# Kernel optimization log

Measured on AMD Instinct MI355X. Metric: run time of the kernel, lower is better.

## Reference

```python
import jax, jax.numpy as jnp
import numpy as np

NH, NKV, HD = 8, 1, 256
EPS = 1e-6
SCALE = 1.0 / np.sqrt(HD)


def _rmsnorm(x, w, eps=EPS):
    # Gemma-style: normalize in fp32, scale by raw weight
    xf = x.astype(jnp.float32)
    rms = jax.lax.rsqrt(jnp.mean(xf * xf, axis=-1, keepdims=True) + eps)
    return (xf * rms).astype(x.dtype) * w


def _apply_rope(q, cos, sin):
    # q: (B, H, T, D); cos/sin: (T, D/2)
    half = q.shape[-1] // 2
    q1, q2 = q[..., :half], q[..., half:]
    c = cos[None, None, :, :]
    s = sin[None, None, :, :]
    return jnp.concatenate([q1 * c - q2 * s, q2 * c + q1 * s], axis=-1)


def setup_inputs() -> dict:
    key = jax.random.key(0)
    ks = jax.random.split(key, 8)
    B, T, H = 2, 2048, 1536
    MAXPOS, HALF = 4096, HD // 2
    x = jax.random.normal(ks[0], (B, T, H), dtype=jnp.float32)
    positions = jnp.arange(T, dtype=jnp.int64) if jax.config.jax_enable_x64 else jnp.arange(T, dtype=jnp.int32)
    # real RoPE tables
    inv_freq = 1.0 / (10000.0 ** (np.arange(0, HALF, dtype=np.float32) / HALF))
    ang = np.arange(MAXPOS, dtype=np.float32)[:, None] * inv_freq[None, :]
    cos = jnp.asarray(np.cos(ang))
    sin = jnp.asarray(np.sin(ang))
    # additive causal mask: 0 on/below diag, -1e9 above
    causal_mask = jnp.where(jnp.tril(jnp.ones((T, T), dtype=bool)), 0.0, -1e9).astype(jnp.float32)
    sc = 0.02
    Wq = jax.random.normal(ks[1], (H, NH * HD), dtype=jnp.float32) * sc
    Wk = jax.random.normal(ks[2], (H, NKV * HD), dtype=jnp.float32) * sc
    Wv = jax.random.normal(ks[3], (H, NKV * HD), dtype=jnp.float32) * sc
    Wo = jax.random.normal(ks[4], (NH * HD, H), dtype=jnp.float32) * sc
    q_norm_w = jnp.ones((HD,), dtype=jnp.float32)
    k_norm_w = jnp.ones((HD,), dtype=jnp.float32)
    return {"x": x, "positions": positions, "cos": cos, "sin": sin,
            "causal_mask": causal_mask, "Wq": Wq, "Wk": Wk, "Wv": Wv,
            "Wo": Wo, "q_norm_w": q_norm_w, "k_norm_w": k_norm_w}


def reference(x, positions, cos, sin, causal_mask, Wq, Wk, Wv, Wo, q_norm_w, k_norm_w):
    B, T, _ = x.shape
    q = (x @ Wq).reshape(B, T, NH, HD)
    k = (x @ Wk).reshape(B, T, NKV, HD)
    v = (x @ Wv).reshape(B, T, NKV, HD)
    q = _rmsnorm(q, q_norm_w)
    k = _rmsnorm(k, k_norm_w)
    q = q.transpose(0, 2, 1, 3)  # (B, NH, T, HD)
    k = k.transpose(0, 2, 1, 3)  # (B, NKV, T, HD)
    v = v.transpose(0, 2, 1, 3)
    cos_pos = cos[positions]
    sin_pos = sin[positions]
    q = _apply_rope(q, cos_pos, sin_pos)
    k = _apply_rope(k, cos_pos, sin_pos)
    if NH != NKV:
        n_rep = NH // NKV
        k = jnp.repeat(k, n_rep, axis=1)
        v = jnp.repeat(v, n_rep, axis=1)
    attn = jnp.einsum('bhqd,bhkd->bhqk', q, k) * SCALE
    attn = attn + causal_mask[None, None]
    attn = jax.nn.softmax(attn, axis=-1)
    out = jnp.einsum('bhqk,bhkd->bhqd', attn, v)
    out = out.transpose(0, 2, 1, 3).reshape(B, T, NH * HD)
    return out @ Wo
```

## Files before the change

### kernel.cpp

```cpp
#include <hip/hip_runtime.h>
#include <hip/hip_bf16.h>

typedef __bf16 bf16x8 __attribute__((ext_vector_type(8)));
typedef float  f32x4  __attribute__((ext_vector_type(4)));

__device__ __forceinline__ f32x4 mfma16(bf16x8 a, bf16x8 b, f32x4 c) {
    return __builtin_amdgcn_mfma_f32_16x16x32_bf16(a, b, c, 0, 0, 0);
}

__device__ __forceinline__ void gload_lds16(const void* g, void* l) {
    __builtin_amdgcn_global_load_lds(
        (const __attribute__((address_space(1))) void*)g,
        (__attribute__((address_space(3))) void*)l, 16, 0, 0);
}

__device__ __forceinline__ float bf2f(unsigned short u) {
    unsigned int x = (unsigned int)u << 16;
    return __builtin_bit_cast(float, x);
}
__device__ __forceinline__ unsigned short f2bf(float f) {
    return __builtin_bit_cast(unsigned short, __float2bfloat16(f));
}

#define B_   2
#define T_   2048
#define H_   1536
#define NH_  8
#define HD_  256
#define ND_  2048
#define NQKV 2560

__global__ __launch_bounds__(256) void cvt_f32_bf16(
        const float* __restrict__ src, __hip_bfloat16* __restrict__ dst, int n8) {
    int i = blockIdx.x * 256 + threadIdx.x;
    if (i >= n8) return;
    const float4* s4 = reinterpret_cast<const float4*>(src) + (size_t)i * 2;
    float4 a = s4[0], b = s4[1];
    short4 o0, o1;
    o0.x = (short)f2bf(a.x); o0.y = (short)f2bf(a.y);
    o0.z = (short)f2bf(a.z); o0.w = (short)f2bf(a.w);
    o1.x = (short)f2bf(b.x); o1.y = (short)f2bf(b.y);
    o1.z = (short)f2bf(b.z); o1.w = (short)f2bf(b.w);
    short4* d4 = reinterpret_cast<short4*>(dst) + (size_t)i * 2;
    d4[0] = o0; d4[1] = o1;
}

__global__ __launch_bounds__(256) void transpose_f32_bf16(
        const float* __restrict__ src, __hip_bfloat16* __restrict__ dst,
        int R, int C) {
    __shared__ float tile[32][33];
    int c0 = blockIdx.x * 32, r0 = blockIdx.y * 32;
    int tx = threadIdx.x & 31, ty = threadIdx.x >> 5;
#pragma unroll
    for (int i = 0; i < 32; i += 8)
        tile[ty + i][tx] = src[(size_t)(r0 + ty + i) * C + c0 + tx];
    __syncthreads();
#pragma unroll
    for (int i = 0; i < 32; i += 8)
        dst[(size_t)(c0 + ty + i) * R + r0 + tx] = __float2bfloat16(tile[tx][ty + i]);
}

__global__ __launch_bounds__(256) void transpose_bf16_s(
        const __hip_bfloat16* __restrict__ src, __hip_bfloat16* __restrict__ dst,
        int R, int C, int ss) {
    __shared__ __hip_bfloat16 tile[32][33];
    int c0 = blockIdx.x * 32, r0 = blockIdx.y * 32;
    int tx = threadIdx.x & 31, ty = threadIdx.x >> 5;
#pragma unroll
    for (int i = 0; i < 32; i += 8)
        tile[ty + i][tx] = src[(size_t)(r0 + ty + i) * ss + c0 + tx];
    __syncthreads();
#pragma unroll
    for (int i = 0; i < 32; i += 8)
        dst[(size_t)(c0 + ty + i) * R + r0 + tx] = tile[tx][ty + i];
}

template <bool F32OUT>
__global__ __launch_bounds__(256) void gemm_bt(
        const __hip_bfloat16* __restrict__ A, const __hip_bfloat16* __restrict__ Bt,
        void* __restrict__ Cp, int M, int N, int K) {
    __shared__ char smem[32768];
    const int tid  = threadIdx.x;
    const int lane = tid & 63;
    const int w    = tid >> 6;
    const int wm   = w >> 1, wn = w & 1;
    const int m0   = blockIdx.y * 128, n0 = blockIdx.x * 128;

    f32x4 acc[4][4] = {};

    auto STAGE = [&](int bsel, int k0) {
        char* As = smem + bsel * 16384;
        char* Bs = As + 8192;
#pragma unroll
        for (int it = 0; it < 2; ++it) {
            int o   = it * 4096 + tid * 16;
            int row = o >> 6;
            int cb  = (o & 63) ^ (((o >> 7) & 3) << 4);
            gload_lds16(A  + (size_t)(m0 + row) * K + k0 + (cb >> 1),
                        As + it * 4096 + w * 1024);
            gload_lds16(Bt + (size_t)(n0 + row) * K + k0 + (cb >> 1),
                        Bs + it * 4096 + w * 1024);
        }
    };

    const int nk = K >> 5;
    STAGE(0, 0);
    for (int ik = 0; ik < nk; ++ik) {
        if (ik + 1 < nk) {
            STAGE((ik + 1) & 1, (ik + 1) << 5);
            asm volatile("s_waitcnt vmcnt(4)" ::: "memory");
        } else {
            asm volatile("s_waitcnt vmcnt(0)" ::: "memory");
        }
        __builtin_amdgcn_s_barrier();
        __builtin_amdgcn_sched_barrier(0);

        const char* As = smem + (ik & 1) * 16384;
        const char* Bs = As + 8192;

        bf16x8 af[4], bfr[4];
#pragma unroll
        for (int i = 0; i < 4; ++i) {
            int ar = wm * 64 + i * 16 + (lane & 15);
            int q  = ar * 64 + ((lane >> 4) << 4);
            af[i]  = *(const bf16x8*)(As + (q ^ (((q >> 7) & 3) << 4)));
            int br = wn * 64 + i * 16 + (lane & 15);
            int p  = br * 64 + ((lane >> 4) << 4);
            bfr[i] = *(const bf16x8*)(Bs + (p ^ (((p >> 7) & 3) << 4)));
        }
#pragma unroll
        for (int i = 0; i < 4; ++i)
#pragma unroll
            for (int j = 0; j < 4; ++j)
                acc[i][j] = mfma16(af[i], bfr[j], acc[i][j]);

        if (ik + 1 < nk) __builtin_amdgcn_s_barrier();
    }

#pragma unroll
    for (int i = 0; i < 4; ++i) {
        int rbase = m0 + wm * 64 + i * 16 + ((lane >> 4) << 2);
#pragma unroll
        for (int j = 0; j < 4; ++j) {
            int col = n0 + wn * 64 + j * 16 + (lane & 15);
#pragma unroll
            for (int r = 0; r < 4; ++r) {
                if (F32OUT)
                    ((float*)Cp)[(size_t)(rbase + r) * N + col] = acc[i][j][r];
                else
                    ((__hip_bfloat16*)Cp)[(size_t)(rbase + r) * N + col] =
                        __float2bfloat16(acc[i][j][r]);
            }
        }
    }
}

__global__ __launch_bounds__(256) void norm_rope(
        const __hip_bfloat16* __restrict__ QKV,
        const float* __restrict__ cosT, const float* __restrict__ sinT,
        const int* __restrict__ positions,
        const float* __restrict__ qw, const float* __restrict__ kw,
        __hip_bfloat16* __restrict__ Qn, __hip_bfloat16* __restrict__ Kn) {
    int gw   = blockIdx.x * 4 + (threadIdx.x >> 6);
    int lane = threadIdx.x & 63;
    int bt   = gw / 9;
    int r    = gw - bt * 9;
    int b    = bt >> 11, t = bt & 2047;

    const __hip_bfloat16* src = QKV + (size_t)bt * NQKV + (r < 8 ? r * HD_ : ND_);
    const float* w;
    __hip_bfloat16* dst;
    float sc;
    if (r < 8) {
        w   = qw;
        dst = Qn + (((size_t)(b * NH_ + r) * T_) + t) * HD_;
        sc  = 0.0901684400555590f;
    } else {
        w   = kw;
        dst = Kn + (size_t)bt * HD_;
        sc  = 1.0f;
    }

    short4 raw = *reinterpret_cast<const short4*>(src + lane * 4);
    float v[4];
    v[0] = bf2f((unsigned short)raw.x); v[1] = bf2f((unsigned short)raw.y);
    v[2] = bf2f((unsigned short)raw.z); v[3] = bf2f((unsigned short)raw.w);

    float ss = v[0]*v[0] + v[1]*v[1] + v[2]*v[2] + v[3]*v[3];
#pragma unroll
    for (int d = 1; d < 64; d <<= 1) ss += __shfl_xor(ss, d);
    float rms = rsqrtf(ss * (1.0f / HD_) + 1e-6f);

    int pos = positions[t];
    float4 c4 = *reinterpret_cast<const float4*>(cosT + (size_t)pos * 128 + (lane & 31) * 4);
    float4 s4 = *reinterpret_cast<const float4*>(sinT + (size_t)pos * 128 + (lane & 31) * 4);
    float cv[4] = { c4.x, c4.y, c4.z, c4.w };
    float sv[4] = { s4.x, s4.y, s4.z, s4.w };

    float4 w4 = *reinterpret_cast<const float4*>(w + lane * 4);
    float wv[4] = { w4.x, w4.y, w4.z, w4.w };

    float nf[4], out[4];
#pragma unroll
    for (int j = 0; j < 4; ++j) nf[j] = v[j] * rms * wv[j];
#pragma unroll
    for (int j = 0; j < 4; ++j) {
        float pf = __shfl_xor(nf[j], 32);
        out[j] = (lane < 32) ? (nf[j] * cv[j] - pf * sv[j])
                             : (nf[j] * cv[j] + pf * sv[j]);
    }
    short4 o4;
    o4.x = (short)f2bf(out[0] * sc); o4.y = (short)f2bf(out[1] * sc);
    o4.z = (short)f2bf(out[2] * sc); o4.w = (short)f2bf(out[3] * sc);
    *reinterpret_cast<short4*>(dst + lane * 4) = o4;
}

#define NPAIR 40
__global__ __launch_bounds__(512) void flash_attn_split(
        const __hip_bfloat16* __restrict__ Qn, const __hip_bfloat16* __restrict__ Kn,
        const __hip_bfloat16* __restrict__ Vt,
        __hip_bfloat16* __restrict__ Opart, float* __restrict__ ml) {
    __shared__ char smem[2 * 16384 + 2 * 16384 + 8 * 1536];
    char* Ps = smem + 65536;

    const int tid = threadIdx.x, lane = tid & 63, wid = tid >> 6;
    const int p = blockIdx.x, bh = blockIdx.y;
    const int b = bh >> 3;

    int qt, c;
    if (p < 4)       { qt = p;                   c = 0; }
    else if (p < 12) { qt = 4 + ((p - 4) >> 1);  c = (p - 4) & 1; }
    else if (p < 24) { qt = 8 + (p - 12) / 3;    c = (p - 12) % 3; }
    else             { qt = 12 + ((p - 24) >> 2); c = (p - 24) & 3; }

    const int kv0 = c * 512;
    const int kv1 = min(kv0 + 512, (qt + 1) * 128);
    const int q0  = qt * 128 + wid * 16;
    const int nst = (kv1 - kv0) >> 5;

    const __hip_bfloat16* Qbase = Qn + ((size_t)bh * T_ + q0) * HD_;
    const __hip_bfloat16* Kb    = Kn + (size_t)b * T_ * HD_;
    const __hip_bfloat16* Vb    = Vt + (size_t)b * HD_ * T_;

    bf16x8 qf[8];
#pragma unroll
    for (int ks = 0; ks < 8; ++ks)
        qf[ks] = *(const bf16x8*)(Qbase + (size_t)(lane & 15) * HD_ + ks * 32 +
                                  ((lane >> 4) << 3));

    bf16x8 onesf;
    {
        __bf16 one = (__bf16)1.0f, zro = (__bf16)0.0f;
        __bf16 val = ((lane & 15) == 0) ? one : zro;
#pragma unroll
        for (int i = 0; i < 8; ++i) onesf[i] = val;
    }

    f32x4 acc[16] = {};
    f32x4 accl = {};

    auto STAGE = [&](int bsel, int kbb) {
        char* Kd = smem + bsel * 16384;
        char* Vd = smem + 32768 + bsel * 16384;
#pragma unroll
        for (int it = 0; it < 2; ++it) {
            int o = it * 8192 + tid * 16;
            {
                int row = o >> 9;
                int cb  = (o & 511) ^ ((row & 31) << 4);
                gload_lds16(Kb + (size_t)(kbb + row) * HD_ + (cb >> 1),
                            Kd + it * 8192 + wid * 1024);
            }
            {
                int row = o >> 6;
                int cb  = (o & 63) ^ (((o >> 7) & 3) << 4);
                gload_lds16(Vb + (size_t)row * T_ + kbb + (cb >> 1),
                            Vd + it * 8192 + wid * 1024);
            }
        }
    };

    STAGE(0, kv0);
    for (int i = 0; i < nst; ++i) {
        const int kb = kv0 + (i << 5);
        if (i + 1 < nst) {
            STAGE((i + 1) & 1, kb + 32);
            asm volatile("s_waitcnt vmcnt(4)" ::: "memory");
        } else {
            asm volatile("s_waitcnt vmcnt(0)" ::: "memory");
        }
        __builtin_amdgcn_s_barrier();
        __builtin_amdgcn_sched_barrier(0);

        const char* Ksb = smem + (i & 1) * 16384;
        const char* Vsb = smem + 32768 + (i & 1) * 16384;

        f32x4 s[2] = {};
        __builtin_amdgcn_s_setprio(1);
#pragma unroll
        for (int cf = 0; cf < 2; ++cf) {
#pragma unroll
            for (int ks = 0; ks < 8; ++ks) {
                int krow = cf * 16 + (lane & 15);
                int q    = krow * 512 + ks * 64 + ((lane >> 4) << 4);
                int sw   = q ^ (((q >> 9) & 31) << 4);
                bf16x8 kf = *(const bf16x8*)(Ksb + sw);
                s[cf] = mfma16(qf[ks], kf, s[cf]);
            }
        }
        __builtin_amdgcn_s_setprio(0);

        const bool nm = (kb + 31 > q0);
        __hip_bfloat16* pw = (__hip_bfloat16*)(Ps + wid * 1536);
#pragma unroll
        for (int r = 0; r < 4; ++r) {
            int rw = ((lane >> 4) << 2) + r;
            float s0 = s[0][r], s1 = s[1][r];
            if (nm) {
                int qrow = q0 + rw;
                if (kb + (lane & 15) > qrow)      s0 = -1e30f;
                if (kb + 16 + (lane & 15) > qrow) s1 = -1e30f;
            }
            pw[rw * 48 + (lane & 15)]      = __float2bfloat16(exp2f(s0));
            pw[rw * 48 + 16 + (lane & 15)] = __float2bfloat16(exp2f(s1));
        }

        bf16x8 pf = *(const bf16x8*)(Ps + wid * 1536 + (lane & 15) * 96 +
                                     ((lane >> 4) << 4));
        __builtin_amdgcn_s_setprio(1);
        accl = mfma16(pf, onesf, accl);
#pragma unroll
        for (int nf = 0; nf < 16; ++nf) {
            int vrow = nf * 16 + (lane & 15);
            int q    = vrow * 64 + ((lane >> 4) << 4);
            int sw   = q ^ (((q >> 7) & 3) << 4);
            bf16x8 vf = *(const bf16x8*)(Vsb + sw);
            acc[nf] = mfma16(pf, vf, acc[nf]);
        }
        __builtin_amdgcn_s_setprio(0);

        if (i + 1 < nst) __builtin_amdgcn_s_barrier();
    }

    const int slot = bh * NPAIR + p;
    __hip_bfloat16* ob = Opart + (size_t)slot * (128 * 256);
#pragma unroll
    for (int r = 0; r < 4; ++r) {
        int rw = wid * 16 + ((lane >> 4) << 2) + r;
        __hip_bfloat16* orow = ob + (size_t)rw * 256;
#pragma unroll
        for (int nf = 0; nf < 16; ++nf)
            orow[nf * 16 + (lane & 15)] = __float2bfloat16(acc[nf][r]);
        if ((lane & 15) == 0) ml[slot * 128 + rw] = accl[r];
    }
}

__global__ __launch_bounds__(256) void attn_combine(
        const __hip_bfloat16* __restrict__ Opart, const float* __restrict__ ml,
        __hip_bfloat16* __restrict__ Obuf) {
    const int bid = blockIdx.x;
    const int bh = bid >> 4, qt = bid & 15;
    const int b = bh >> 3, h = bh & 7;

    int ps, np;
    if (qt < 4)       { ps = qt;                 np = 1; }
    else if (qt < 8)  { ps = 4 + 2 * (qt - 4);   np = 2; }
    else if (qt < 12) { ps = 12 + 3 * (qt - 8);  np = 3; }
    else              { ps = 24 + 4 * (qt - 12); np = 4; }
    const int slot0 = bh * NPAIR + ps;

    const int t = threadIdx.x;
    const int row = t >> 1, half = t & 1;

    float L = 0.0f;
    for (int i = 0; i < np; ++i) L += ml[(slot0 + i) * 128 + row];
    float rL = 1.0f / L;

    __hip_bfloat16* orow = Obuf + ((size_t)(b * T_ + qt * 128 + row)) * ND_ +
                           h * HD_ + half * 128;
#pragma unroll
    for (int cc = 0; cc < 16; ++cc) {
        float a[8] = {0,0,0,0,0,0,0,0};
        for (int i = 0; i < np; ++i) {
            const __hip_bfloat16* pr = Opart + (size_t)(slot0 + i) * (128 * 256) +
                                       (size_t)row * 256 + half * 128 + cc * 8;
            short4 v0 = *reinterpret_cast<const short4*>(pr);
            short4 v1 = *reinterpret_cast<const short4*>(pr + 4);
            a[0] += bf2f((unsigned short)v0.x);
            a[1] += bf2f((unsigned short)v0.y);
            a[2] += bf2f((unsigned short)v0.z);
            a[3] += bf2f((unsigned short)v0.w);
            a[4] += bf2f((unsigned short)v1.x);
            a[5] += bf2f((unsigned short)v1.y);
            a[6] += bf2f((unsigned short)v1.z);
            a[7] += bf2f((unsigned short)v1.w);
        }
        short4 o0, o1;
        o0.x = (short)f2bf(a[0] * rL); o0.y = (short)f2bf(a[1] * rL);
        o0.z = (short)f2bf(a[2] * rL); o0.w = (short)f2bf(a[3] * rL);
        o1.x = (short)f2bf(a[4] * rL); o1.y = (short)f2bf(a[5] * rL);
        o1.z = (short)f2bf(a[6] * rL); o1.w = (short)f2bf(a[7] * rL);
        *reinterpret_cast<short4*>(orow + cc * 8)     = o0;
        *reinterpret_cast<short4*>(orow + cc * 8 + 4) = o1;
    }
}

extern "C" void kernel_launch(void* const* d_in, const int* in_sizes, int n_in,
                              void* d_out, int out_size, void* d_ws, size_t ws_size,
                              hipStream_t stream) {
    const float* x    = (const float*)d_in[0];
    const int*   pos  = (const int*)d_in[1];
    const float* cosT = (const float*)d_in[2];
    const float* sinT = (const float*)d_in[3];
    const float* Wq = (const float*)d_in[5];
    const float* Wk = (const float*)d_in[6];
    const float* Wv = (const float*)d_in[7];
    const float* Wo = (const float*)d_in[8];
    const float* qw = (const float*)d_in[9];
    const float* kw = (const float*)d_in[10];

    char* ws0 = (char*)d_ws;
    __hip_bfloat16* WqkvT  = (__hip_bfloat16*)(ws0 + 0);
    __hip_bfloat16* xb     = (__hip_bfloat16*)(ws0 + 7864320);
    __hip_bfloat16* QKVraw = (__hip_bfloat16*)(ws0 + 20447232);
    __hip_bfloat16* Opart  = (__hip_bfloat16*)(ws0 + 0);
    float*          ml     = (float*)(ws0 + 41943040);
    __hip_bfloat16* WoT    = (__hip_bfloat16*)(ws0 + 42598400);
    __hip_bfloat16* Qn     = (__hip_bfloat16*)(ws0 + 48889856);
    __hip_bfloat16* Obuf   = Qn;
    __hip_bfloat16* Kn     = (__hip_bfloat16*)(ws0 + 65667072);
    __hip_bfloat16* Vt     = (__hip_bfloat16*)(ws0 + 67764224);
    float* out = (float*)d_out;

    const int MT = B_ * T_;

    cvt_f32_bf16<<<(MT * H_ / 8 + 255) / 256, 256, 0, stream>>>(x, xb, MT * H_ / 8);

    transpose_f32_bf16<<<dim3(ND_ / 32, H_ / 32), 256, 0, stream>>>(
        Wq, WqkvT, H_, ND_);
    transpose_f32_bf16<<<dim3(HD_ / 32, H_ / 32), 256, 0, stream>>>(
        Wk, WqkvT + (size_t)ND_ * H_, H_, HD_);
    transpose_f32_bf16<<<dim3(HD_ / 32, H_ / 32), 256, 0, stream>>>(
        Wv, WqkvT + (size_t)(ND_ + HD_) * H_, H_, HD_);
    transpose_f32_bf16<<<dim3(H_ / 32, ND_ / 32), 256, 0, stream>>>(
        Wo, WoT, ND_, H_);

    gemm_bt<false><<<dim3(NQKV / 128, MT / 128), 256, 0, stream>>>(
        xb, WqkvT, QKVraw, MT, NQKV, H_);

    norm_rope<<<(MT * 9) / 4, 256, 0, stream>>>(
        QKVraw, cosT, sinT, pos, qw, kw, Qn, Kn);

    for (int b = 0; b < B_; ++b)
        transpose_bf16_s<<<dim3(HD_ / 32, T_ / 32), 256, 0, stream>>>(
            QKVraw + (size_t)b * T_ * NQKV + ND_ + HD_,
            Vt + (size_t)b * HD_ * T_, T_, HD_, NQKV);

    flash_attn_split<<<dim3(NPAIR, B_ * NH_), 512, 0, stream>>>(
        Qn, Kn, Vt, Opart, ml);
    attn_combine<<<B_ * NH_ * 16, 256, 0, stream>>>(Opart, ml, Obuf);

    gemm_bt<true><<<dim3(H_ / 128, MT / 128), 256, 0, stream>>>(
        Obuf, WoT, out, MT, H_, ND_);
}
```

Baseline: 241.3 us.

## Give each attention wave 32 query rows to reuse K/V LDS fragments

The flash attention kernel goes from 8 waves of 16 query rows to 4 waves of 32 query rows per block. Each K and V fragment read from LDS now feeds two MFMAs, which halves LDS read traffic per MFMA. The staging loop issues twice as many loads per thread and the wait count is raised to match. This raises register pressure (a doubled accumulator array), and fewer waves per block may reduce latency hiding; launch bounds are set to 256 threads with 2 blocks per CU.

```diff
diff --git a/kernel.cpp b/kernel.cpp
--- a/kernel.cpp
+++ b/kernel.cpp
@@ -216,11 +216,11 @@
 }
 
 #define NPAIR 40
-__global__ __launch_bounds__(512) void flash_attn_split(
+__global__ __launch_bounds__(256, 2) void flash_attn_split(
         const __hip_bfloat16* __restrict__ Qn, const __hip_bfloat16* __restrict__ Kn,
         const __hip_bfloat16* __restrict__ Vt,
         __hip_bfloat16* __restrict__ Opart, float* __restrict__ ml) {
-    __shared__ char smem[2 * 16384 + 2 * 16384 + 8 * 1536];
+    __shared__ char smem[2 * 16384 + 2 * 16384 + 4 * 3072];
     char* Ps = smem + 65536;
 
     const int tid = threadIdx.x, lane = tid & 63, wid = tid >> 6;
@@ -235,18 +235,21 @@
 
     const int kv0 = c * 512;
     const int kv1 = min(kv0 + 512, (qt + 1) * 128);
-    const int q0  = qt * 128 + wid * 16;
+    const int q0  = qt * 128 + wid * 32;
     const int nst = (kv1 - kv0) >> 5;
 
     const __hip_bfloat16* Qbase = Qn + ((size_t)bh * T_ + q0) * HD_;
     const __hip_bfloat16* Kb    = Kn + (size_t)b * T_ * HD_;
     const __hip_bfloat16* Vb    = Vt + (size_t)b * HD_ * T_;
 
-    bf16x8 qf[8];
-#pragma unroll
-    for (int ks = 0; ks < 8; ++ks)
-        qf[ks] = *(const bf16x8*)(Qbase + (size_t)(lane & 15) * HD_ + ks * 32 +
-                                  ((lane >> 4) << 3));
+    bf16x8 qf[2][8];
+#pragma unroll
+    for (int rf = 0; rf < 2; ++rf)
+#pragma unroll
+        for (int ks = 0; ks < 8; ++ks)
+            qf[rf][ks] = *(const bf16x8*)(Qbase +
+                (size_t)(rf * 16 + (lane & 15)) * HD_ + ks * 32 +
+                ((lane >> 4) << 3));
 
     bf16x8 onesf;
     {
@@ -256,26 +259,26 @@
         for (int i = 0; i < 8; ++i) onesf[i] = val;
     }
 
-    f32x4 acc[16] = {};
-    f32x4 accl = {};
+    f32x4 acc[2][16] = {};
+    f32x4 accl[2] = {};
 
     auto STAGE = [&](int bsel, int kbb) {
         char* Kd = smem + bsel * 16384;
         char* Vd = smem + 32768 + bsel * 16384;
 #pragma unroll
-        for (int it = 0; it < 2; ++it) {
-            int o = it * 8192 + tid * 16;
+        for (int it = 0; it < 4; ++it) {
+            int o = it * 4096 + tid * 16;
             {
                 int row = o >> 9;
                 int cb  = (o & 511) ^ ((row & 31) << 4);
                 gload_lds16(Kb + (size_t)(kbb + row) * HD_ + (cb >> 1),
-                            Kd + it * 8192 + wid * 1024);
+                            Kd + it * 4096 + wid * 1024);
             }
             {
                 int row = o >> 6;
                 int cb  = (o & 63) ^ (((o >> 7) & 3) << 4);
                 gload_lds16(Vb + (size_t)row * T_ + kbb + (cb >> 1),
-                            Vd + it * 8192 + wid * 1024);
+                            Vd + it * 4096 + wid * 1024);
             }
         }
     };
@@ -285,7 +288,7 @@
         const int kb = kv0 + (i << 5);
         if (i + 1 < nst) {
             STAGE((i + 1) & 1, kb + 32);
-            asm volatile("s_waitcnt vmcnt(4)" ::: "memory");
+            asm volatile("s_waitcnt vmcnt(8)" ::: "memory");
         } else {
             asm volatile("s_waitcnt vmcnt(0)" ::: "memory");
         }
@@ -295,7 +298,7 @@
         const char* Ksb = smem + (i & 1) * 16384;
         const char* Vsb = smem + 32768 + (i & 1) * 16384;
 
-        f32x4 s[2] = {};
+        f32x4 s[2][2] = {};
         __builtin_amdgcn_s_setprio(1);
 #pragma unroll
         for (int cf = 0; cf < 2; ++cf) {
@@ -305,37 +308,44 @@
                 int q    = krow * 512 + ks * 64 + ((lane >> 4) << 4);
                 int sw   = q ^ (((q >> 9) & 31) << 4);
                 bf16x8 kf = *(const bf16x8*)(Ksb + sw);
-                s[cf] = mfma16(qf[ks], kf, s[cf]);
+                s[0][cf] = mfma16(qf[0][ks], kf, s[0][cf]);
+                s[1][cf] = mfma16(qf[1][ks], kf, s[1][cf]);
             }
         }
         __builtin_amdgcn_s_setprio(0);
 
         const bool nm = (kb + 31 > q0);
-        __hip_bfloat16* pw = (__hip_bfloat16*)(Ps + wid * 1536);
-#pragma unroll
-        for (int r = 0; r < 4; ++r) {
-            int rw = ((lane >> 4) << 2) + r;
-            float s0 = s[0][r], s1 = s[1][r];
-            if (nm) {
-                int qrow = q0 + rw;
-                if (kb + (lane & 15) > qrow)      s0 = -1e30f;
-                if (kb + 16 + (lane & 15) > qrow) s1 = -1e30f;
+        __hip_bfloat16* pw = (__hip_bfloat16*)(Ps + wid * 3072);
+#pragma unroll
+        for (int rf = 0; rf < 2; ++rf)
+#pragma unroll
+            for (int r = 0; r < 4; ++r) {
+                int rw = rf * 16 + ((lane >> 4) << 2) + r;
+                float s0 = s[rf][0][r], s1 = s[rf][1][r];
+                if (nm) {
+                    int qrow = q0 + rw;
+                    if (kb + (lane & 15) > qrow)      s0 = -1e30f;
+                    if (kb + 16 + (lane & 15) > qrow) s1 = -1e30f;
+                }
+                pw[rw * 48 + (lane & 15)]      = __float2bfloat16(exp2f(s0));
+                pw[rw * 48 + 16 + (lane & 15)] = __float2bfloat16(exp2f(s1));
             }
-            pw[rw * 48 + (lane & 15)]      = __float2bfloat16(exp2f(s0));
-            pw[rw * 48 + 16 + (lane & 15)] = __float2bfloat16(exp2f(s1));
-        }
-
-        bf16x8 pf = *(const bf16x8*)(Ps + wid * 1536 + (lane & 15) * 96 +
-                                     ((lane >> 4) << 4));
+
+        bf16x8 pf0 = *(const bf16x8*)(Ps + wid * 3072 +
+                                      (size_t)(lane & 15) * 96 + ((lane >> 4) << 4));
+        bf16x8 pf1 = *(const bf16x8*)(Ps + wid * 3072 +
+                                      (size_t)(16 + (lane & 15)) * 96 + ((lane >> 4) << 4));
         __builtin_amdgcn_s_setprio(1);
-        accl = mfma16(pf, onesf, accl);
+        accl[0] = mfma16(pf0, onesf, accl[0]);
+        accl[1] = mfma16(pf1, onesf, accl[1]);
 #pragma unroll
         for (int nf = 0; nf < 16; ++nf) {
             int vrow = nf * 16 + (lane & 15);
             int q    = vrow * 64 + ((lane >> 4) << 4);
             int sw   = q ^ (((q >> 7) & 3) << 4);
             bf16x8 vf = *(const bf16x8*)(Vsb + sw);
-            acc[nf] = mfma16(pf, vf, acc[nf]);
+            acc[0][nf] = mfma16(pf0, vf, acc[0][nf]);
+            acc[1][nf] = mfma16(pf1, vf, acc[1][nf]);
         }
         __builtin_amdgcn_s_setprio(0);
 
@@ -345,14 +355,16 @@
     const int slot = bh * NPAIR + p;
     __hip_bfloat16* ob = Opart + (size_t)slot * (128 * 256);
 #pragma unroll
-    for (int r = 0; r < 4; ++r) {
-        int rw = wid * 16 + ((lane >> 4) << 2) + r;
-        __hip_bfloat16* orow = ob + (size_t)rw * 256;
-#pragma unroll
-        for (int nf = 0; nf < 16; ++nf)
-            orow[nf * 16 + (lane & 15)] = __float2bfloat16(acc[nf][r]);
-        if ((lane & 15) == 0) ml[slot * 128 + rw] = accl[r];
-    }
+    for (int rf = 0; rf < 2; ++rf)
+#pragma unroll
+        for (int r = 0; r < 4; ++r) {
+            int rw = wid * 32 + rf * 16 + ((lane >> 4) << 2) + r;
+            __hip_bfloat16* orow = ob + (size_t)rw * 256;
+#pragma unroll
+            for (int nf = 0; nf < 16; ++nf)
+                orow[nf * 16 + (lane & 15)] = __float2bfloat16(acc[rf][nf][r]);
+            if ((lane & 15) == 0) ml[slot * 128 + rw] = accl[rf][r];
+        }
 }
 
 __global__ __launch_bounds__(256) void attn_combine(
@@ -456,7 +468,7 @@
             QKVraw + (size_t)b * T_ * NQKV + ND_ + HD_,
             Vt + (size_t)b * HD_ * T_, T_, HD_, NQKV);
 
-    flash_attn_split<<<dim3(NPAIR, B_ * NH_), 512, 0, stream>>>(
+    flash_attn_split<<<dim3(NPAIR, B_ * NH_), 256, 0, stream>>>(
         Qn, Kn, Vt, Opart, ml);
     attn_combine<<<B_ * NH_ * 16, 256, 0, stream>>>(Opart, ml, Obuf);
 
```

Result: slower. 371.1 us (+53.8%).
